# Performance work log

Hardware: AMD Instinct MI355X
Metric: run time of the kernel (lower is better)

Reference implementation:

```python
import jax, jax.numpy as jnp
import numpy as np
import math

N_CHANNELS = 256
D_K = 64
N_HEADS = N_CHANNELS // D_K  # 4
N_GROUPS = 32
EPS = 1e-5
SCALE = 1.0 / math.sqrt(math.sqrt(D_K))


def setup_inputs() -> dict:
    key = jax.random.key(0)
    ks = jax.random.split(key, 7)
    B, C, H, W = 2, N_CHANNELS, 64, 64
    inner = N_HEADS * D_K
    x = jax.random.normal(ks[0], (B, C, H, W), dtype=jnp.float32)
    gn_w = jnp.ones((C,), dtype=jnp.float32)
    gn_b = jnp.zeros((C,), dtype=jnp.float32)
    proj_w = jax.random.normal(ks[1], (3 * inner, C), dtype=jnp.float32) / math.sqrt(C)
    proj_b = jnp.zeros((3 * inner,), dtype=jnp.float32)
    out_w = jax.random.normal(ks[2], (C, inner), dtype=jnp.float32) / math.sqrt(inner)
    out_b = jnp.zeros((C,), dtype=jnp.float32)
    return {"x": x, "gn_w": gn_w, "gn_b": gn_b, "proj_w": proj_w,
            "proj_b": proj_b, "out_w": out_w, "out_b": out_b}


def _group_norm(x, gamma, beta):
    # x: [B, C, H, W], 32 groups, affine per channel
    B, C, H, W = x.shape
    xg = x.reshape(B, N_GROUPS, C // N_GROUPS, H * W)
    mean = xg.mean(axis=(2, 3), keepdims=True)
    var = xg.var(axis=(2, 3), keepdims=True)
    xn = (xg - mean) * jax.lax.rsqrt(var + EPS)
    xn = xn.reshape(B, C, H, W)
    return xn * gamma[None, :, None, None] + beta[None, :, None, None]


def reference(x, gn_w, gn_b, proj_w, proj_b, out_w, out_b):
    B, C, H, W = x.shape
    S = H * W
    h = _group_norm(x, gn_w, gn_b).reshape(B, C, S).transpose(0, 2, 1)  # [B, S, C]
    qkv = h @ proj_w.T + proj_b                                          # [B, S, 3*nh*dk]
    qkv = qkv.reshape(B, S, N_HEADS, 3 * D_K)
    q, k, v = jnp.split(qkv, 3, axis=-1)                                 # [B, S, nh, dk] each
    # bihd,bjhd->bijh with scale applied to both q and k (net 1/sqrt(dk))
    attn = jnp.einsum('bihd,bjhd->bijh', q * SCALE, k * SCALE)
    attn = jax.nn.softmax(attn, axis=2)
    res = jnp.einsum('bijh,bjhd->bihd', attn, v).reshape(B, S, N_HEADS * D_K)
    res = res @ out_w.T + out_b                                          # [B, S, C]
    res = res.transpose(0, 2, 1).reshape(B, C, H, W)
    return res + x
```

## Files before the change

kernel.cpp:

```cpp
#include <hip/hip_runtime.h>
#include <math.h>

#define NB 2
#define NC 256
#define NS 4096
#define NG 32
#define CPG 8
#define NH 4
#define DK 64
#define NQKV 768
#define NKG 4
#define TPG 16
#define QS 0.18033688011112042f

typedef __attribute__((ext_vector_type(8))) short short8;
typedef __attribute__((ext_vector_type(4))) float f32x4;
typedef __attribute__((ext_vector_type(16))) float f32x16;
typedef __attribute__((ext_vector_type(4))) unsigned uint4v;

union U8 { uint4v u; short8 s; };

__device__ __forceinline__ short f2bf(float f){
  union { float f; unsigned u; } v; v.f = f;
  unsigned r = v.u + 0x7fffu + ((v.u >> 16) & 1u);
  return (short)(r >> 16);
}
__device__ __forceinline__ float ex2(float x){
  float y; asm("v_exp_f32 %0, %1" : "=v"(y) : "v"(x)); return y;
}
__device__ __forceinline__ unsigned cvtpk(float lo, float hi){
  unsigned u; asm("v_cvt_pk_bf16_f32 %0, %1, %2" : "=v"(u) : "v"(lo), "v"(hi)); return u;
}
__device__ __forceinline__ void pl32swap(unsigned &x, unsigned &y){
  asm("v_permlane32_swap_b32 %0, %1" : "+v"(x), "+v"(y));
}

__global__ __launch_bounds__(256) void k_prep(const float* __restrict__ x,
                                              const float* __restrict__ pw,
                                              const float* __restrict__ ow,
                                              const float* __restrict__ gw,
                                              const float* __restrict__ gb,
                                              short* __restrict__ h,
                                              short* __restrict__ pwb,
                                              short* __restrict__ owb){
  int bk = blockIdx.x;
  int tid = threadIdx.x;
  if (bk < 64){
    int b = bk >> 5, g = bk & 31;
    const float* base = x + (size_t)bk*(CPG*NS);
    const f32x4* b4 = (const f32x4*)base;
    float s = 0.f, ss = 0.f;
    for (int i = tid; i < (CPG*NS)/4; i += 256){
      f32x4 v = b4[i];
      s  += (v[0]+v[1])+(v[2]+v[3]);
      ss += (v[0]*v[0]+v[1]*v[1])+(v[2]*v[2]+v[3]*v[3]);
    }
    for (int o = 32; o > 0; o >>= 1){ s += __shfl_down(s,o); ss += __shfl_down(ss,o); }
    __shared__ float red[8];
    __shared__ float mrs[2];
    int w = tid >> 6;
    if ((tid & 63) == 0){ red[w] = s; red[4+w] = ss; }
    __syncthreads();
    if (tid == 0){
      float S  = red[0]+red[1]+red[2]+red[3];
      float SS = red[4]+red[5]+red[6]+red[7];
      const float inv = 1.f/(float)(CPG*NS);
      float m = S*inv; float var = SS*inv - m*m;
      mrs[0] = m; mrs[1] = rsqrtf(var + 1e-5f);
    }
    __syncthreads();
    float mu = mrs[0], rs = mrs[1];
    float wv[8], bv[8];
    #pragma unroll
    for (int c = 0; c < 8; ++c){
      wv[c] = gw[g*8 + c] * rs;
      bv[c] = gb[g*8 + c] - mu * wv[c];
    }
    short* hb = h + (size_t)b*NS*NC + g*8;
    for (int i = tid; i < NS; i += 256){
      unsigned u[4];
      #pragma unroll
      for (int c2 = 0; c2 < 4; ++c2){
        float v0 = base[(size_t)(2*c2  )*NS + i]*wv[2*c2  ] + bv[2*c2  ];
        float v1 = base[(size_t)(2*c2+1)*NS + i]*wv[2*c2+1] + bv[2*c2+1];
        u[c2] = cvtpk(v0, v1);
      }
      *(uint4v*)&hb[(size_t)i*NC] = (uint4v){u[0],u[1],u[2],u[3]};
    }
  } else {
    int i = (bk - 64)*256 + tid;
    if (i < NQKV*NC) pwb[i] = f2bf(pw[i]);
    if (i < NC*NC)   owb[i] = f2bf(ow[i]);
  }
}

__global__ __launch_bounds__(256) void k_qkv(const short* __restrict__ h,
                                             const short* __restrict__ wb,
                                             const float* __restrict__ pb,
                                             short* __restrict__ qo,
                                             short* __restrict__ ko,
                                             short* __restrict__ vto){
  __shared__ short As[64][72];
  __shared__ short Bs[128][72];
  int m0 = blockIdx.x << 6;
  int n0 = blockIdx.y << 7;
  int tid = threadIdx.x;
  int lane = tid & 63, wid = tid >> 6;
  int wm = (wid >> 1) << 5, wn = (wid & 1) << 6;
  int l15 = lane & 15, lg = lane >> 4;
  const f32x4 fz = {0.f,0.f,0.f,0.f};
  f32x4 acc[2][4];
  for (int i=0;i<2;i++) for(int j=0;j<4;j++) acc[i][j] = fz;
  for (int k0 = 0; k0 < NC; k0 += 64){
    __syncthreads();
    for (int it = 0; it < 2; ++it){
      int c = it*256 + tid;
      int r = c >> 3, ch = (c & 7) << 3;
      *(short8*)&As[r][ch] = *(const short8*)&h[((size_t)(m0 + r))*NC + k0 + ch];
    }
    for (int it = 0; it < 4; ++it){
      int c = it*256 + tid;
      int r = c >> 3, ch = (c & 7) << 3;
      *(short8*)&Bs[r][ch] = *(const short8*)&wb[((size_t)(n0 + r))*NC + k0 + ch];
    }
    __syncthreads();
    #pragma unroll
    for (int kk = 0; kk < 2; ++kk){
      short8 a[2], b[4];
      for (int mf=0; mf<2; ++mf) a[mf] = *(const short8*)&As[wm + mf*16 + l15][kk*32 + lg*8];
      for (int nf=0; nf<4; ++nf) b[nf] = *(const short8*)&Bs[wn + nf*16 + l15][kk*32 + lg*8];
      for (int mf=0; mf<2; ++mf)
        for (int nf=0; nf<4; ++nf)
          acc[mf][nf] = __builtin_amdgcn_mfma_f32_16x16x32_bf16(a[mf], b[nf], acc[mf][nf], 0,0,0);
    }
  }
  for (int mf=0; mf<2; ++mf)
    for (int nf=0; nf<4; ++nf)
      for (int r=0; r<4; ++r){
        int m = m0 + wm + mf*16 + lg*4 + r;
        int o = n0 + wn + nf*16 + l15;
        float val = acc[mf][nf][r] + pb[o];
        int b_ = m >> 12, s = m & 4095;
        int hh = o / 192, rem = o - hh*192;
        int t = rem >> 6, d = rem & 63;
        size_t bh = (size_t)(b_*NH + hh);
        if (t == 0)      qo [(bh*NS + s)*DK + d] = f2bf(val * QS);
        else if (t == 1) ko [(bh*NS + s)*DK + d] = f2bf(val);
        else             vto[(bh*DK + d)*NS + s] = f2bf(val);
      }
}

struct SMK { short kv[NKG][2][2][64][72]; };
struct SMC {
  float gOB[3][4][64][33];
  float ml[3][4][2][32];
  float fOB[4][64][33];
};

__global__ __launch_bounds__(1024, 4) void k_attn(const short* __restrict__ q,
                                                  const short* __restrict__ k,
                                                  const short* __restrict__ vt,
                                                  short* __restrict__ ao){
  extern __shared__ char smem[];
  SMK* sk = (SMK*)smem;
  SMC* sc = (SMC*)smem;

  int blk = blockIdx.x;
  int bh = blk & 7;
  int q0 = (blk >> 3) << 7;
  const short* Qb = q  + (size_t)bh*NS*DK;
  const short* Kb = k  + (size_t)bh*NS*DK;
  const short* Vb = vt + (size_t)bh*DK*NS;
  int tid = threadIdx.x, lane = tid & 63, wid = tid >> 6;
  int l31 = lane & 31, hi = lane >> 5;
  int g = wid >> 2, wq = wid & 3;
  int gtid = tid & 255;
  int kvbase = g << 10;

  short8 bq[4];
  {
    const short* qrow = Qb + (size_t)(q0 + wq*32 + l31)*DK + hi*8;
    #pragma unroll
    for (int s2 = 0; s2 < 4; ++s2) bq[s2] = *(const short8*)(qrow + s2*16);
  }

  f32x16 ot0, ot1;
  #pragma unroll
  for (int i = 0; i < 16; ++i){ ot0[i] = 0.f; ot1[i] = 0.f; }
  float mrun = -1e30f, lrun = 0.f;

  short8 kpre[2], vpre[2];
  #pragma unroll
  for (int it = 0; it < 2; ++it){
    int c = it*256 + gtid, r = c >> 3, col = (c & 7) << 3;
    kpre[it] = *(const short8*)&Kb[(size_t)(kvbase + r)*DK + col];
    vpre[it] = *(const short8*)&Vb[(size_t)r*NS + kvbase + col];
  }
  #pragma unroll
  for (int it = 0; it < 2; ++it){
    int c = it*256 + gtid, r = c >> 3, col = (c & 7) << 3;
    *(short8*)&sk->kv[g][0][0][r][col] = kpre[it];
    *(short8*)&sk->kv[g][0][1][r][col] = vpre[it];
  }
  #pragma unroll
  for (int it = 0; it < 2; ++it){
    int c = it*256 + gtid, r = c >> 3, col = (c & 7) << 3;
    kpre[it] = *(const short8*)&Kb[(size_t)(kvbase + 64 + r)*DK + col];
    vpre[it] = *(const short8*)&Vb[(size_t)r*NS + kvbase + 64 + col];
  }

  for (int t = 0; t < TPG; ++t){
    __syncthreads();
    const short (*Kl)[72] = sk->kv[g][t & 1][0];
    const short (*Vl)[72] = sk->kv[g][t & 1][1];
    f32x16 st0, st1;
    #pragma unroll
    for (int i = 0; i < 16; ++i){ st0[i] = 0.f; st1[i] = 0.f; }
    const short* Kr0 = &Kl[l31][hi*8];
    const short* Kr1 = &Kl[32 + l31][hi*8];
    #pragma unroll
    for (int s2 = 0; s2 < 4; ++s2){
      short8 ka0 = *(const short8*)(Kr0 + s2*16);
      short8 ka1 = *(const short8*)(Kr1 + s2*16);
      st0 = __builtin_amdgcn_mfma_f32_32x32x16_bf16(ka0, bq[s2], st0, 0,0,0);
      st1 = __builtin_amdgcn_mfma_f32_32x32x16_bf16(ka1, bq[s2], st1, 0,0,0);
    }
    if (t + 1 < TPG){
      int nb = (t + 1) & 1;
      #pragma unroll
      for (int it = 0; it < 2; ++it){
        int c = it*256 + gtid, r = c >> 3, col = (c & 7) << 3;
        *(short8*)&sk->kv[g][nb][0][r][col] = kpre[it];
        *(short8*)&sk->kv[g][nb][1][r][col] = vpre[it];
      }
    }
    if (t + 2 < TPG){
      int kv0 = kvbase + (t + 2)*64;
      #pragma unroll
      for (int it = 0; it < 2; ++it){
        int c = it*256 + gtid, r = c >> 3, col = (c & 7) << 3;
        kpre[it] = *(const short8*)&Kb[(size_t)(kv0 + r)*DK + col];
        vpre[it] = *(const short8*)&Vb[(size_t)r*NS + kv0 + col];
      }
    }
    float mx = -1e30f;
    #pragma unroll
    for (int i = 0; i < 16; ++i) mx = fmaxf(mx, fmaxf(st0[i], st1[i]));
    mx = fmaxf(mx, __shfl_xor(mx, 32));
    if (!__all(mx - mrun <= 8.f)){
      float mnew = fmaxf(mrun, mx);
      float corr = ex2(mrun - mnew);
      lrun *= corr;
      #pragma unroll
      for (int i = 0; i < 16; ++i){ ot0[i] *= corr; ot1[i] *= corr; }
      mrun = mnew;
    }
    float p0[16], p1[16]; float ps = 0.f;
    #pragma unroll
    for (int i = 0; i < 16; ++i){
      p0[i] = ex2(st0[i] - mrun); p1[i] = ex2(st1[i] - mrun);
      ps += p0[i] + p1[i];
    }
    ps += __shfl_xor(ps, 32);
    lrun += ps;
    unsigned pk0[8], pk1[8];
    #pragma unroll
    for (int a = 0; a < 4; ++a){
      pk0[a]     = cvtpk(p0[4*a+0], p0[4*a+1]);
      pk1[a]     = cvtpk(p0[4*a+2], p0[4*a+3]);
      pk0[4 + a] = cvtpk(p1[4*a+0], p1[4*a+1]);
      pk1[4 + a] = cvtpk(p1[4*a+2], p1[4*a+3]);
    }
    const short* Vr0 = &Vl[l31][hi*8];
    const short* Vr1 = &Vl[32 + l31][hi*8];
    #pragma unroll
    for (int i2 = 0; i2 < 4; ++i2){
      unsigned w0 = pk0[2*i2], w2 = pk0[2*i2+1]; pl32swap(w0, w2);
      unsigned w1 = pk1[2*i2], w3 = pk1[2*i2+1]; pl32swap(w1, w3);
      U8 cv; cv.u = (uint4v){w0, w1, w2, w3};
      short8 av0 = *(const short8*)(Vr0 + i2*16);
      short8 av1 = *(const short8*)(Vr1 + i2*16);
      ot0 = __builtin_amdgcn_mfma_f32_32x32x16_bf16(av0, cv.s, ot0, 0,0,0);
      ot1 = __builtin_amdgcn_mfma_f32_32x32x16_bf16(av1, cv.s, ot1, 0,0,0);
    }
  }

  __syncthreads();
  if (g > 0){
    #pragma unroll
    for (int r2 = 0; r2 < 16; ++r2){
      int dl = (r2 & 3) + 8*(r2 >> 2) + 4*hi;
      sc->gOB[g-1][wq][dl][l31]      = ot0[r2];
      sc->gOB[g-1][wq][32 + dl][l31] = ot1[r2];
    }
    if (hi == 0){ sc->ml[g-1][wq][0][l31] = mrun; sc->ml[g-1][wq][1][l31] = lrun; }
  }
  __syncthreads();
  if (g == 0){
    float m1 = sc->ml[0][wq][0][l31], l1 = sc->ml[0][wq][1][l31];
    float m2 = sc->ml[1][wq][0][l31], l2 = sc->ml[1][wq][1][l31];
    float m3 = sc->ml[2][wq][0][l31], l3 = sc->ml[2][wq][1][l31];
    float M  = fmaxf(fmaxf(mrun, m1), fmaxf(m2, m3));
    float w0 = ex2(mrun - M), w1 = ex2(m1 - M), w2 = ex2(m2 - M), w3 = ex2(m3 - M);
    float inv = 1.f/(lrun*w0 + l1*w1 + l2*w2 + l3*w3);
    w0 *= inv; w1 *= inv; w2 *= inv; w3 *= inv;
    #pragma unroll
    for (int r2 = 0; r2 < 16; ++r2){
      int dl = (r2 & 3) + 8*(r2 >> 2) + 4*hi;
      sc->fOB[wq][dl][l31] = ot0[r2]*w0 + sc->gOB[0][wq][dl][l31]*w1
                           + sc->gOB[1][wq][dl][l31]*w2 + sc->gOB[2][wq][dl][l31]*w3;
      sc->fOB[wq][32+dl][l31] = ot1[r2]*w0 + sc->gOB[0][wq][32+dl][l31]*w1
                              + sc->gOB[1][wq][32+dl][l31]*w2 + sc->gOB[2][wq][32+dl][l31]*w3;
    }
  }
  __syncthreads();
  {
    int ql = tid >> 3, dc = (tid & 7) << 3;
    int b_ = bh >> 2, hh = bh & 3;
    float v2[8];
    #pragma unroll
    for (int i = 0; i < 8; ++i) v2[i] = sc->fOB[ql >> 5][dc + i][ql & 31];
    uint4v wa = { cvtpk(v2[0],v2[1]), cvtpk(v2[2],v2[3]),
                  cvtpk(v2[4],v2[5]), cvtpk(v2[6],v2[7]) };
    size_t base = ((size_t)b_*NS + q0 + ql)*NC + hh*DK + dc;
    *(uint4v*)&ao[base] = wa;
  }
}

__global__ __launch_bounds__(256) void k_out(const short* __restrict__ aoin,
                                             const short* __restrict__ wb,
                                             const float* __restrict__ ob,
                                             const float* __restrict__ x,
                                             float* __restrict__ out){
  __shared__ short As[64][40];
  __shared__ short Bs[64][40];
  int m0 = blockIdx.x << 6;
  int n0 = blockIdx.y << 6;
  int tid = threadIdx.x;
  int lane = tid & 63, wid = tid >> 6;
  int wm = (wid >> 1) << 5, wn = (wid & 1) << 5;
  int l15 = lane & 15, lg = lane >> 4;
  const f32x4 fz = {0.f,0.f,0.f,0.f};
  f32x4 acc[2][2];
  for (int i=0;i<2;i++) for(int j=0;j<2;j++) acc[i][j] = fz;
  for (int k0 = 0; k0 < NC; k0 += 32){
    __syncthreads();
    {
      int c = tid;
      int r = c >> 2, kk8 = (c & 3) << 3;
      *(short8*)&As[r][kk8] = *(const short8*)&aoin[((size_t)(m0 + r))*NC + k0 + kk8];
      *(short8*)&Bs[r][kk8] = *(const short8*)&wb  [((size_t)(n0 + r))*NC + k0 + kk8];
    }
    __syncthreads();
    short8 a[2], b[2];
    for (int mf=0; mf<2; ++mf) a[mf] = *(const short8*)&As[wm + mf*16 + l15][lg*8];
    for (int nf=0; nf<2; ++nf) b[nf] = *(const short8*)&Bs[wn + nf*16 + l15][lg*8];
    for (int mf=0; mf<2; ++mf)
      for (int nf=0; nf<2; ++nf)
        acc[mf][nf] = __builtin_amdgcn_mfma_f32_16x16x32_bf16(a[mf], b[nf], acc[mf][nf], 0,0,0);
  }
  for (int mf=0; mf<2; ++mf)
    for (int nf=0; nf<2; ++nf)
      for (int r=0; r<4; ++r){
        int m = m0 + wm + mf*16 + lg*4 + r;
        int o = n0 + wn + nf*16 + l15;
        int b_ = m >> 12, s = m & 4095;
        size_t idx = ((size_t)b_*NC + o)*NS + s;
        out[idx] = acc[mf][nf][r] + ob[o] + x[idx];
      }
}

extern "C" void kernel_launch(void* const* d_in, const int* in_sizes, int n_in,
                              void* d_out, int out_size, void* d_ws, size_t ws_size,
                              hipStream_t stream){
  const float* x   = (const float*)d_in[0];
  const float* gnw = (const float*)d_in[1];
  const float* gnb = (const float*)d_in[2];
  const float* pw  = (const float*)d_in[3];
  const float* pb  = (const float*)d_in[4];
  const float* ow  = (const float*)d_in[5];
  const float* ob  = (const float*)d_in[6];
  float* out = (float*)d_out;

  char* ws = (char*)d_ws;
  short* wqkv = (short*)(ws + 512);
  short* wout = wqkv + NQKV*NC;
  short* h    = wout + NC*NC;
  short* qb   = h   + (size_t)NB*NS*NC;
  short* kb   = qb  + (size_t)NB*NH*NS*DK;
  short* vtb  = kb  + (size_t)NB*NH*NS*DK;
  short* ao   = vtb + (size_t)NB*NH*NS*DK;

  k_prep<<<832, 256, 0, stream>>>(x, pw, ow, gnw, gnb, h, wqkv, wout);
  k_qkv<<<dim3(128, 6), 256, 0, stream>>>(h, wqkv, pb, qb, kb, vtb);
  k_attn<<<256, 1024, sizeof(SMK), stream>>>(qb, kb, vtb, ao);
  k_out<<<dim3(128, 4), 256, 0, stream>>>(ao, wout, ob, x, out);
}
```

Measured before the change: 99.17 us.

## Split group-norm into atomic stats and apply kernels; tree-reduce softmax max and sum

The single prep kernel, which ran only 64 blocks for the group-norm, is split in two. A stats kernel with 256 blocks reduces quarter-groups and atomically accumulates sums into a zeroed buffer. An apply kernel with 1024 blocks then normalises quarter-slices and converts the weights to bf16. Separately, the attention kernel's per-tile max and sum reductions become tree reductions to shorten the serial dependency chain. The cost is an extra memset and kernel launch, a second read of x, and float atomics that make the statistics order-nondeterministic.

```diff
diff --git a/kernel.cpp b/kernel.cpp
--- a/kernel.cpp
+++ b/kernel.cpp
@@ -35,41 +35,50 @@
   asm("v_permlane32_swap_b32 %0, %1" : "+v"(x), "+v"(y));
 }
 
-__global__ __launch_bounds__(256) void k_prep(const float* __restrict__ x,
-                                              const float* __restrict__ pw,
-                                              const float* __restrict__ ow,
-                                              const float* __restrict__ gw,
-                                              const float* __restrict__ gb,
-                                              short* __restrict__ h,
-                                              short* __restrict__ pwb,
-                                              short* __restrict__ owb){
-  int bk = blockIdx.x;
+__global__ __launch_bounds__(256) void k_stats(const float* __restrict__ x,
+                                               float* __restrict__ sbuf){
+  int blk = blockIdx.x;
+  int bg = blk >> 2, qt = blk & 3;
+  const float* base = x + (size_t)bg*(CPG*NS) + (size_t)qt*(CPG*NS/4);
+  const f32x4* b4 = (const f32x4*)base;
+  float s = 0.f, ss = 0.f;
+  #pragma unroll
+  for (int it = 0; it < 8; ++it){
+    f32x4 v = b4[it*256 + threadIdx.x];
+    s  += (v[0]+v[1])+(v[2]+v[3]);
+    ss += (v[0]*v[0]+v[1]*v[1])+(v[2]*v[2]+v[3]*v[3]);
+  }
+  for (int o = 32; o > 0; o >>= 1){ s += __shfl_down(s,o); ss += __shfl_down(ss,o); }
+  __shared__ float red[8];
+  int w = threadIdx.x >> 6;
+  if ((threadIdx.x & 63) == 0){ red[w] = s; red[4+w] = ss; }
+  __syncthreads();
+  if (threadIdx.x == 0){
+    float S  = red[0]+red[1]+red[2]+red[3];
+    float SS = red[4]+red[5]+red[6]+red[7];
+    atomicAdd(&sbuf[bg], S);
+    atomicAdd(&sbuf[64 + bg], SS);
+  }
+}
+
+__global__ __launch_bounds__(256) void k_apply(const float* __restrict__ x,
+                                               const float* __restrict__ sbuf,
+                                               const float* __restrict__ gw,
+                                               const float* __restrict__ gb,
+                                               const float* __restrict__ pw,
+                                               const float* __restrict__ ow,
+                                               short* __restrict__ h,
+                                               short* __restrict__ pwb,
+                                               short* __restrict__ owb){
+  int blk = blockIdx.x;
   int tid = threadIdx.x;
-  if (bk < 64){
-    int b = bk >> 5, g = bk & 31;
-    const float* base = x + (size_t)bk*(CPG*NS);
-    const f32x4* b4 = (const f32x4*)base;
-    float s = 0.f, ss = 0.f;
-    for (int i = tid; i < (CPG*NS)/4; i += 256){
-      f32x4 v = b4[i];
-      s  += (v[0]+v[1])+(v[2]+v[3]);
-      ss += (v[0]*v[0]+v[1]*v[1])+(v[2]*v[2]+v[3]*v[3]);
-    }
-    for (int o = 32; o > 0; o >>= 1){ s += __shfl_down(s,o); ss += __shfl_down(ss,o); }
-    __shared__ float red[8];
-    __shared__ float mrs[2];
-    int w = tid >> 6;
-    if ((tid & 63) == 0){ red[w] = s; red[4+w] = ss; }
-    __syncthreads();
-    if (tid == 0){
-      float S  = red[0]+red[1]+red[2]+red[3];
-      float SS = red[4]+red[5]+red[6]+red[7];
-      const float inv = 1.f/(float)(CPG*NS);
-      float m = S*inv; float var = SS*inv - m*m;
-      mrs[0] = m; mrs[1] = rsqrtf(var + 1e-5f);
-    }
-    __syncthreads();
-    float mu = mrs[0], rs = mrs[1];
+  if (blk < 256){
+    int bg = blk >> 2, qt = blk & 3;
+    int b = bg >> 5, g = bg & 31;
+    const float* base = x + (size_t)bg*(CPG*NS);
+    const float inv = 1.f/(float)(CPG*NS);
+    float mu = sbuf[bg]*inv;
+    float rs = rsqrtf(sbuf[64+bg]*inv - mu*mu + 1e-5f);
     float wv[8], bv[8];
     #pragma unroll
     for (int c = 0; c < 8; ++c){
@@ -77,7 +86,10 @@
       bv[c] = gb[g*8 + c] - mu * wv[c];
     }
     short* hb = h + (size_t)b*NS*NC + g*8;
-    for (int i = tid; i < NS; i += 256){
+    int s0 = qt << 10;
+    #pragma unroll
+    for (int it = 0; it < 4; ++it){
+      int i = s0 + it*256 + tid;
       unsigned u[4];
       #pragma unroll
       for (int c2 = 0; c2 < 4; ++c2){
@@ -88,7 +100,7 @@
       *(uint4v*)&hb[(size_t)i*NC] = (uint4v){u[0],u[1],u[2],u[3]};
     }
   } else {
-    int i = (bk - 64)*256 + tid;
+    int i = (blk - 256)*256 + tid;
     if (i < NQKV*NC) pwb[i] = f2bf(pw[i]);
     if (i < NC*NC)   owb[i] = f2bf(ow[i]);
   }
@@ -243,10 +255,14 @@
         vpre[it] = *(const short8*)&Vb[(size_t)r*NS + kv0 + col];
       }
     }
-    float mx = -1e30f;
-    #pragma unroll
-    for (int i = 0; i < 16; ++i) mx = fmaxf(mx, fmaxf(st0[i], st1[i]));
-    mx = fmaxf(mx, __shfl_xor(mx, 32));
+    float tm[16];
+    #pragma unroll
+    for (int i = 0; i < 16; ++i) tm[i] = fmaxf(st0[i], st1[i]);
+    #pragma unroll
+    for (int s2 = 8; s2 > 0; s2 >>= 1)
+      #pragma unroll
+      for (int i = 0; i < s2; ++i) tm[i] = fmaxf(tm[i], tm[i+s2]);
+    float mx = fmaxf(tm[0], __shfl_xor(tm[0], 32));
     if (!__all(mx - mrun <= 8.f)){
       float mnew = fmaxf(mrun, mx);
       float corr = ex2(mrun - mnew);
@@ -255,14 +271,19 @@
       for (int i = 0; i < 16; ++i){ ot0[i] *= corr; ot1[i] *= corr; }
       mrun = mnew;
     }
-    float p0[16], p1[16]; float ps = 0.f;
+    float p0[16], p1[16];
     #pragma unroll
     for (int i = 0; i < 16; ++i){
       p0[i] = ex2(st0[i] - mrun); p1[i] = ex2(st1[i] - mrun);
-      ps += p0[i] + p1[i];
-    }
-    ps += __shfl_xor(ps, 32);
-    lrun += ps;
+    }
+    float tu[16];
+    #pragma unroll
+    for (int i = 0; i < 16; ++i) tu[i] = p0[i] + p1[i];
+    #pragma unroll
+    for (int s2 = 8; s2 > 0; s2 >>= 1)
+      #pragma unroll
+      for (int i = 0; i < s2; ++i) tu[i] += tu[i+s2];
+    lrun += tu[0] + __shfl_xor(tu[0], 32);
     unsigned pk0[8], pk1[8];
     #pragma unroll
     for (int a = 0; a < 4; ++a){
@@ -383,6 +404,7 @@
   float* out = (float*)d_out;
 
   char* ws = (char*)d_ws;
+  float* sbuf = (float*)ws;
   short* wqkv = (short*)(ws + 512);
   short* wout = wqkv + NQKV*NC;
   short* h    = wout + NC*NC;
@@ -391,7 +413,9 @@
   short* vtb  = kb  + (size_t)NB*NH*NS*DK;
   short* ao   = vtb + (size_t)NB*NH*NS*DK;
 
-  k_prep<<<832, 256, 0, stream>>>(x, pw, ow, gnw, gnb, h, wqkv, wout);
+  hipMemsetAsync(sbuf, 0, 512, stream);
+  k_stats<<<256, 256, 0, stream>>>(x, sbuf);
+  k_apply<<<1024, 256, 0, stream>>>(x, sbuf, gnw, gnb, pw, ow, h, wqkv, wout);
   k_qkv<<<dim3(128, 6), 256, 0, stream>>>(h, wqkv, pb, qb, kb, vtb);
   k_attn<<<256, 1024, sizeof(SMK), stream>>>(qb, kb, vtb, ao);
   k_out<<<dim3(128, 4), 256, 0, stream>>>(ao, wout, ob, x, out);
```

Measured after the change: 92.33 us. -6.9%, faster.

## Split group-norm across 256 blocks with cooperative grid sync and LDS staging

Applied to the files above, without the earlier changes.

The prep kernel now splits each batch-group's group-norm over four blocks instead of one. Each block stages its slice of x in shared memory, accumulates partial sums with global atomics, and waits at a cooperative grid.sync before normalizing from LDS rather than re-reading global memory. Weight conversion to bf16 is vectorized to four elements per thread with packed converts. This raises parallelism and removes a second pass over x, at the cost of a memset, a cooperative launch and a grid-wide barrier.

```diff
diff --git a/kernel.cpp b/kernel.cpp
--- a/kernel.cpp
+++ b/kernel.cpp
@@ -1,5 +1,8 @@
 #include <hip/hip_runtime.h>
+#include <hip/hip_cooperative_groups.h>
 #include <math.h>
+
+namespace cg = cooperative_groups;
 
 #define NB 2
 #define NC 256
@@ -16,6 +19,7 @@
 typedef __attribute__((ext_vector_type(8))) short short8;
 typedef __attribute__((ext_vector_type(4))) float f32x4;
 typedef __attribute__((ext_vector_type(16))) float f32x16;
+typedef __attribute__((ext_vector_type(2))) unsigned uint2v;
 typedef __attribute__((ext_vector_type(4))) unsigned uint4v;
 
 union U8 { uint4v u; short8 s; };
@@ -35,41 +39,49 @@
   asm("v_permlane32_swap_b32 %0, %1" : "+v"(x), "+v"(y));
 }
 
-__global__ __launch_bounds__(256) void k_prep(const float* __restrict__ x,
-                                              const float* __restrict__ pw,
-                                              const float* __restrict__ ow,
-                                              const float* __restrict__ gw,
-                                              const float* __restrict__ gb,
-                                              short* __restrict__ h,
-                                              short* __restrict__ pwb,
-                                              short* __restrict__ owb){
-  int bk = blockIdx.x;
-  int tid = threadIdx.x;
-  if (bk < 64){
-    int b = bk >> 5, g = bk & 31;
-    const float* base = x + (size_t)bk*(CPG*NS);
-    const f32x4* b4 = (const f32x4*)base;
+__global__ __launch_bounds__(256) void k_gn(const float* __restrict__ x,
+                                            float* __restrict__ sbuf,
+                                            const float* __restrict__ gw,
+                                            const float* __restrict__ gb,
+                                            const float* __restrict__ pw,
+                                            const float* __restrict__ ow,
+                                            short* __restrict__ h,
+                                            short* __restrict__ pwb,
+                                            short* __restrict__ owb){
+  cg::grid_group grid = cg::this_grid();
+  __shared__ float xs[8][1024];
+  __shared__ float red[8];
+  __shared__ float mrs[2];
+  int blk = blockIdx.x, tid = threadIdx.x;
+  if (blk < 256){
+    int bg = blk >> 2, qt = blk & 3;
+    int b = bg >> 5, g = bg & 31;
+    const float* base = x + (size_t)bg*(CPG*NS) + qt*1024;
     float s = 0.f, ss = 0.f;
-    for (int i = tid; i < (CPG*NS)/4; i += 256){
-      f32x4 v = b4[i];
+    #pragma unroll
+    for (int c = 0; c < 8; ++c){
+      f32x4 v = *(const f32x4*)&base[(size_t)c*NS + tid*4];
+      *(f32x4*)&xs[c][tid*4] = v;
       s  += (v[0]+v[1])+(v[2]+v[3]);
       ss += (v[0]*v[0]+v[1]*v[1])+(v[2]*v[2]+v[3]*v[3]);
     }
     for (int o = 32; o > 0; o >>= 1){ s += __shfl_down(s,o); ss += __shfl_down(ss,o); }
-    __shared__ float red[8];
-    __shared__ float mrs[2];
     int w = tid >> 6;
     if ((tid & 63) == 0){ red[w] = s; red[4+w] = ss; }
     __syncthreads();
     if (tid == 0){
-      float S  = red[0]+red[1]+red[2]+red[3];
-      float SS = red[4]+red[5]+red[6]+red[7];
-      const float inv = 1.f/(float)(CPG*NS);
-      float m = S*inv; float var = SS*inv - m*m;
-      mrs[0] = m; mrs[1] = rsqrtf(var + 1e-5f);
-    }
-    __syncthreads();
-    float mu = mrs[0], rs = mrs[1];
+      atomicAdd(&sbuf[bg],      red[0]+red[1]+red[2]+red[3]);
+      atomicAdd(&sbuf[64 + bg], red[4]+red[5]+red[6]+red[7]);
+    }
+    grid.sync();
+    if (tid == 0){
+      mrs[0] = atomicAdd(&sbuf[bg], 0.f);
+      mrs[1] = atomicAdd(&sbuf[64 + bg], 0.f);
+    }
+    __syncthreads();
+    const float inv = 1.f/(float)(CPG*NS);
+    float mu = mrs[0]*inv;
+    float rs = rsqrtf(mrs[1]*inv - mu*mu + 1e-5f);
     float wv[8], bv[8];
     #pragma unroll
     for (int c = 0; c < 8; ++c){
@@ -77,20 +89,29 @@
       bv[c] = gb[g*8 + c] - mu * wv[c];
     }
     short* hb = h + (size_t)b*NS*NC + g*8;
-    for (int i = tid; i < NS; i += 256){
+    #pragma unroll
+    for (int it = 0; it < 4; ++it){
+      int i = it*256 + tid;
       unsigned u[4];
       #pragma unroll
       for (int c2 = 0; c2 < 4; ++c2){
-        float v0 = base[(size_t)(2*c2  )*NS + i]*wv[2*c2  ] + bv[2*c2  ];
-        float v1 = base[(size_t)(2*c2+1)*NS + i]*wv[2*c2+1] + bv[2*c2+1];
+        float v0 = xs[2*c2  ][i]*wv[2*c2  ] + bv[2*c2  ];
+        float v1 = xs[2*c2+1][i]*wv[2*c2+1] + bv[2*c2+1];
         u[c2] = cvtpk(v0, v1);
       }
-      *(uint4v*)&hb[(size_t)i*NC] = (uint4v){u[0],u[1],u[2],u[3]};
+      *(uint4v*)&hb[(size_t)(qt*1024 + i)*NC] = (uint4v){u[0],u[1],u[2],u[3]};
     }
   } else {
-    int i = (bk - 64)*256 + tid;
-    if (i < NQKV*NC) pwb[i] = f2bf(pw[i]);
-    if (i < NC*NC)   owb[i] = f2bf(ow[i]);
+    int j = (blk - 256)*1024 + tid*4;
+    if (j < NQKV*NC){
+      f32x4 v = *(const f32x4*)&pw[j];
+      *(uint2v*)&pwb[j] = (uint2v){ cvtpk(v[0],v[1]), cvtpk(v[2],v[3]) };
+    } else {
+      int j2 = j - NQKV*NC;
+      f32x4 v = *(const f32x4*)&ow[j2];
+      *(uint2v*)&owb[j2] = (uint2v){ cvtpk(v[0],v[1]), cvtpk(v[2],v[3]) };
+    }
+    grid.sync();
   }
 }
 
@@ -383,6 +404,7 @@
   float* out = (float*)d_out;
 
   char* ws = (char*)d_ws;
+  float* sbuf = (float*)ws;
   short* wqkv = (short*)(ws + 512);
   short* wout = wqkv + NQKV*NC;
   short* h    = wout + NC*NC;
@@ -391,7 +413,12 @@
   short* vtb  = kb  + (size_t)NB*NH*NS*DK;
   short* ao   = vtb + (size_t)NB*NH*NS*DK;
 
-  k_prep<<<832, 256, 0, stream>>>(x, pw, ow, gnw, gnb, h, wqkv, wout);
+  hipMemsetAsync(sbuf, 0, 512, stream);
+  {
+    void* args[] = { (void*)&x, (void*)&sbuf, (void*)&gnw, (void*)&gnb,
+                     (void*)&pw, (void*)&ow, (void*)&h, (void*)&wqkv, (void*)&wout };
+    hipLaunchCooperativeKernel((const void*)k_gn, dim3(512), dim3(256), args, 0, stream);
+  }
   k_qkv<<<dim3(128, 6), 256, 0, stream>>>(h, wqkv, pb, qb, kb, vtb);
   k_attn<<<256, 1024, sizeof(SMK), stream>>>(qb, kb, vtb, ao);
   k_out<<<dim3(128, 4), 256, 0, stream>>>(ao, wout, ob, x, out);
```

New measurement: 156.3 us. 1.58x slower.
